# Optimization experiments

Hardware: AMD Instinct MI355X
Metric: run time of the kernel (lower is better)

Reference implementation:

```python
import jax, jax.numpy as jnp
import numpy as np

RCR, RCA = 5.1, 3.5
ETA_R, ZETA, ETA_A = 19.7, 14.1, 12.5
SHF_R = jnp.asarray((0.8 + 0.26875 * np.arange(16)).astype(np.float32))   # 16 radial shifts
SHF_Z = jnp.asarray(((2 * np.arange(8) + 1) * np.pi / 8).astype(np.float32))  # 8 angle shifts
SHF_A = jnp.asarray((0.8 + 0.3375 * np.arange(8)).astype(np.float32))    # 8 angular-radial shifts
NUM_SPECIES = 7
NUM_PAIRS = NUM_SPECIES * (NUM_SPECIES + 1) // 2  # 28 unordered species pairs
N = 2000          # atoms
K = 24            # max neighbors considered for angular terms (Rca=3.5 -> ~18 at this density)
BOX = 27.1        # (N / 0.1 atoms/A^3)^(1/3)

def _triu_index(n):
    ret = np.zeros((n, n), dtype=np.int32)
    iu = np.triu_indices(n)
    ret[iu] = np.arange(iu[0].size)
    ret[iu[1], iu[0]] = ret[iu]
    return ret
TRIU = jnp.asarray(_triu_index(NUM_SPECIES))  # [7,7] -> pair index in 0..27

def _fc(d, rc):
    # cosine cutoff, zero beyond rc
    return jnp.where(d <= rc, 0.5 * jnp.cos(jnp.pi * d / rc) + 0.5, 0.0)

def setup_inputs():
    key = jax.random.key(0)
    k1, k2 = jax.random.split(key)
    species = jax.random.randint(k1, (N,), 0, NUM_SPECIES)
    positions = jax.random.uniform(k2, (N, 3), dtype=jnp.float32) * BOX
    return {"species": species, "positions": positions}

def _aev_mean(species, positions):
    n = positions.shape[0]
    eye = jnp.eye(n, dtype=bool)
    diff = positions[:, None, :] - positions[None, :, :]          # [n,n,3]
    d2 = jnp.sum(diff * diff, -1)
    dist = jnp.sqrt(jnp.where(eye, 1.0, d2))                      # safe sqrt on diagonal
    dist = jnp.where(eye, 2.0 * RCR, dist)                        # exclude self (fc -> 0)

    # ---- radial AEV: 0.25 * exp(-EtaR (d - ShfR)^2) * fc(d, Rcr), scattered by neighbor species
    fc_r = _fc(dist, RCR)
    rad = 0.25 * jnp.exp(-ETA_R * (dist[..., None] - SHF_R) ** 2) * fc_r[..., None]  # [n,n,16]
    oh = jax.nn.one_hot(species, NUM_SPECIES, dtype=positions.dtype)                  # [n,7]
    radial = jnp.einsum('ijr,js->isr', rad, oh)                   # [n,7,16]

    # ---- angular AEV over triplets (j, i, k) with j,k among K nearest neighbors of i
    neg, idx = jax.lax.top_k(-dist, K)                            # idx: [n,K]
    nd = -neg                                                     # neighbor distances [n,K]
    valid = nd <= RCA
    vec = positions[idx] - positions[:, None, :]                  # [n,K,3]
    rj = nd[:, :, None]
    rk = nd[:, None, :]
    cos_ang = 0.95 * jnp.einsum('nad,nbd->nab', vec, vec) / (rj * rk)  # torchani's 0.95 factor
    theta = jnp.arccos(cos_ang)                                   # [n,K,K]
    f1 = ((1.0 + jnp.cos(theta[..., None] - SHF_Z)) / 2.0) ** ZETA               # [n,K,K,8]
    f2 = jnp.exp(-ETA_A * (((rj + rk) / 2.0)[..., None] - SHF_A) ** 2)           # [n,K,K,8]
    fcj = _fc(nd, RCA)
    tri = jnp.triu(jnp.ones((K, K), dtype=bool), 1)               # unordered pairs j<k
    mask = valid[:, :, None] & valid[:, None, :] & tri
    pref = 2.0 * fcj[:, :, None] * fcj[:, None, :] * mask.astype(positions.dtype)
    g = (f1[..., :, None] * f2[..., None, :]).reshape(n, K, K, 64) * pref[..., None]  # [n,K,K,64]
    sp_nb = species[idx]                                          # [n,K]
    pair_idx = TRIU[sp_nb[:, :, None], sp_nb[:, None, :]]         # [n,K,K] in 0..27
    row = jnp.arange(n)[:, None, None]
    angular = jnp.zeros((n, NUM_PAIRS, 64), dtype=positions.dtype).at[row, pair_idx].add(g)

    aev = jnp.concatenate([radial.reshape(n, -1), angular.reshape(n, -1)], axis=-1)  # [n,1904]
    return jnp.mean(aev)

def reference(species, positions):
    return _aev_mean(species, positions)
```

## Files before the change

kernel.cpp:

```cpp
#include <hip/hip_runtime.h>
#include <math.h>

#define NATOMS   2000
#define KNBR     24
#define CAND_CAP 64
#define BLOCK    256
#define NFEAT    1904.0f

__device__ __forceinline__ float wave_reduce_add(float v) {
    #pragma unroll
    for (int off = 32; off > 0; off >>= 1) v += __shfl_down(v, off, 64);
    return v;
}

__global__ __launch_bounds__(BLOCK) void aev_sum_kernel(
        const float* __restrict__ pos, float* __restrict__ accum) {
    constexpr float RCR = 5.1f, RCA = 3.5f;
    constexpr float ETA_R = 19.7f, ZETA = 14.1f, ETA_A = 12.5f;
    constexpr float PI = 3.14159265358979323846f;

    __shared__ float sx[NATOMS], sy[NATOMS], sz[NATOMS];
    __shared__ float cand_d[CAND_CAP];
    __shared__ int   cand_j[CAND_CAP];
    __shared__ int   s_cnt;
    __shared__ float nbx[KNBR], nby[KNBR], nbz[KNBR], nbd[KNBR], nbfc[KNBR];
    __shared__ float red_r[BLOCK / 64], red_a[BLOCK / 64];

    const int tid = threadIdx.x;
    const int i   = blockIdx.x;

    for (int j = tid; j < NATOMS; j += BLOCK) {
        sx[j] = pos[3 * j + 0];
        sy[j] = pos[3 * j + 1];
        sz[j] = pos[3 * j + 2];
    }
    if (tid == 0) s_cnt = 0;
    __syncthreads();

    const float xi = sx[i], yi = sy[i], zi = sz[i];

    float rsum = 0.0f;
    for (int j = tid; j < NATOMS; j += BLOCK) {
        if (j == i) continue;
        float dx = sx[j] - xi, dy = sy[j] - yi, dz = sz[j] - zi;
        float d2 = dx * dx + dy * dy + dz * dz;
        if (d2 <= RCR * RCR) {
            float d  = sqrtf(d2);
            float fc = 0.5f * __cosf(d * (PI / RCR)) + 0.5f;
            float s  = 0.0f;
            #pragma unroll
            for (int r = 0; r < 16; r++) {
                float t = d - (0.8f + 0.26875f * (float)r);
                s += __expf(-ETA_R * t * t);
            }
            rsum += 0.25f * fc * s;
            if (d2 <= RCA * RCA) {
                int c = atomicAdd(&s_cnt, 1);
                if (c < CAND_CAP) { cand_d[c] = d; cand_j[c] = j; }
            }
        }
    }
    rsum = wave_reduce_add(rsum);
    if ((tid & 63) == 0) red_r[tid >> 6] = rsum;
    __syncthreads();

    int cnt = min(s_cnt, CAND_CAP);
    int M   = min(cnt, KNBR);
    if (tid < cnt) {
        float dt = cand_d[tid];
        int   jt = cand_j[tid];
        int rank = 0;
        for (int u = 0; u < cnt; u++) {
            float du = cand_d[u];
            if (du < dt || (du == dt && cand_j[u] < jt)) rank++;
        }
        if (rank < KNBR) {
            nbx[rank]  = sx[jt] - xi;
            nby[rank]  = sy[jt] - yi;
            nbz[rank]  = sz[jt] - zi;
            nbd[rank]  = dt;
            nbfc[rank] = 0.5f * __cosf(dt * (PI / RCA)) + 0.5f;
        }
    }
    __syncthreads();

    float asum = 0.0f;
    int npairs = M * (M - 1) / 2;
    for (int p = tid; p < npairs; p += BLOCK) {
        int a = 0, rem = p;
        while (rem >= M - 1 - a) { rem -= M - 1 - a; a++; }
        int b = a + 1 + rem;

        float dot = nbx[a] * nbx[b] + nby[a] * nby[b] + nbz[a] * nbz[b];
        float ra = nbd[a], rb = nbd[b];
        float cosang = 0.95f * dot / (ra * rb);
        float theta  = acosf(cosang);

        float f1 = 0.0f;
        #pragma unroll
        for (int z = 0; z < 8; z++) {
            float shz = (2.0f * (float)z + 1.0f) * (PI / 8.0f);
            float c   = 0.5f * (1.0f + __cosf(theta - shz));
            f1 += __powf(fmaxf(c, 1e-20f), ZETA);
        }
        float avg = 0.5f * (ra + rb);
        float f2  = 0.0f;
        #pragma unroll
        for (int s8 = 0; s8 < 8; s8++) {
            float t = avg - (0.8f + 0.3375f * (float)s8);
            f2 += __expf(-ETA_A * t * t);
        }
        asum += 2.0f * nbfc[a] * nbfc[b] * f1 * f2;
    }
    asum = wave_reduce_add(asum);
    if ((tid & 63) == 0) red_a[tid >> 6] = asum;
    __syncthreads();

    if (tid == 0) {
        float total = 0.0f;
        #pragma unroll
        for (int w = 0; w < BLOCK / 64; w++) total += red_r[w] + red_a[w];
        atomicAdd(accum, total);
    }
}

__global__ void finalize_kernel(const float* __restrict__ accum,
                                float* __restrict__ out) {
    out[0] = accum[0] / ((float)NATOMS * NFEAT);
}

extern "C" void kernel_launch(void* const* d_in, const int* in_sizes, int n_in,
                              void* d_out, int out_size, void* d_ws, size_t ws_size,
                              hipStream_t stream) {
    const float* pos = (const float*)d_in[1];
    float* accum = (float*)d_ws;

    hipMemsetAsync(d_ws, 0, sizeof(float), stream);
    aev_sum_kernel<<<NATOMS, BLOCK, 0, stream>>>(pos, accum);
    finalize_kernel<<<1, 1, 0, stream>>>(accum, (float*)d_out);
}
```

Measured before the change: 96.47 us.

## Compact radial hits with wave ballot, drop shared position copy, per-block partials

```diff
diff --git a/kernel.cpp b/kernel.cpp
--- a/kernel.cpp
+++ b/kernel.cpp
@@ -3,7 +3,8 @@
 
 #define NATOMS   2000
 #define KNBR     24
-#define CAND_CAP 64
+#define HCAP     192
+#define ACAP     64
 #define BLOCK    256
 #define NFEAT    1904.0f
 
@@ -13,78 +14,89 @@
     return v;
 }
 
-__global__ __launch_bounds__(BLOCK) void aev_sum_kernel(
-        const float* __restrict__ pos, float* __restrict__ accum) {
+__global__ __launch_bounds__(BLOCK) void aev_block_kernel(
+        const float* __restrict__ pos, float* __restrict__ partial) {
     constexpr float RCR = 5.1f, RCA = 3.5f;
     constexpr float ETA_R = 19.7f, ZETA = 14.1f, ETA_A = 12.5f;
     constexpr float PI = 3.14159265358979323846f;
 
-    __shared__ float sx[NATOMS], sy[NATOMS], sz[NATOMS];
-    __shared__ float cand_d[CAND_CAP];
-    __shared__ int   cand_j[CAND_CAP];
-    __shared__ int   s_cnt;
+    __shared__ float hd2[HCAP];
+    __shared__ int   hj[HCAP];
+    __shared__ float ad[ACAP];
+    __shared__ int   aj[ACAP];
+    __shared__ int   s_hcnt, s_acnt;
     __shared__ float nbx[KNBR], nby[KNBR], nbz[KNBR], nbd[KNBR], nbfc[KNBR];
-    __shared__ float red_r[BLOCK / 64], red_a[BLOCK / 64];
+    __shared__ float red[BLOCK / 64];
 
-    const int tid = threadIdx.x;
-    const int i   = blockIdx.x;
+    const int tid  = threadIdx.x;
+    const int i    = blockIdx.x;
+    const int lane = tid & 63;
 
-    for (int j = tid; j < NATOMS; j += BLOCK) {
-        sx[j] = pos[3 * j + 0];
-        sy[j] = pos[3 * j + 1];
-        sz[j] = pos[3 * j + 2];
-    }
-    if (tid == 0) s_cnt = 0;
+    if (tid == 0) { s_hcnt = 0; s_acnt = 0; }
     __syncthreads();
 
-    const float xi = sx[i], yi = sy[i], zi = sz[i];
+    const float xi = pos[3 * i + 0], yi = pos[3 * i + 1], zi = pos[3 * i + 2];
 
-    float rsum = 0.0f;
-    for (int j = tid; j < NATOMS; j += BLOCK) {
-        if (j == i) continue;
-        float dx = sx[j] - xi, dy = sy[j] - yi, dz = sz[j] - zi;
+    for (int jb = 0; jb < NATOMS; jb += BLOCK) {
+        int j  = jb + tid;
+        int jc = j < NATOMS ? j : NATOMS - 1;
+        float dx = pos[3 * jc + 0] - xi;
+        float dy = pos[3 * jc + 1] - yi;
+        float dz = pos[3 * jc + 2] - zi;
         float d2 = dx * dx + dy * dy + dz * dz;
-        if (d2 <= RCR * RCR) {
-            float d  = sqrtf(d2);
-            float fc = 0.5f * __cosf(d * (PI / RCR)) + 0.5f;
-            float s  = 0.0f;
-            #pragma unroll
-            for (int r = 0; r < 16; r++) {
-                float t = d - (0.8f + 0.26875f * (float)r);
-                s += __expf(-ETA_R * t * t);
-            }
-            rsum += 0.25f * fc * s;
-            if (d2 <= RCA * RCA) {
-                int c = atomicAdd(&s_cnt, 1);
-                if (c < CAND_CAP) { cand_d[c] = d; cand_j[c] = j; }
-            }
+        bool hit = (j < NATOMS) && (j != i) && (d2 <= RCR * RCR);
+        unsigned long long m = __ballot(hit);
+        int nw   = __popcll(m);
+        int base = 0;
+        if (lane == 0 && nw) base = atomicAdd(&s_hcnt, nw);
+        base = __shfl(base, 0, 64);
+        if (hit) {
+            int idx = base + __popcll(m & ((1ull << lane) - 1ull));
+            if (idx < HCAP) { hd2[idx] = d2; hj[idx] = j; }
         }
     }
-    rsum = wave_reduce_add(rsum);
-    if ((tid & 63) == 0) red_r[tid >> 6] = rsum;
     __syncthreads();
 
-    int cnt = min(s_cnt, CAND_CAP);
+    float psum = 0.0f;
+    int hcnt = min(s_hcnt, HCAP);
+    for (int c = tid; c < hcnt; c += BLOCK) {
+        float d2 = hd2[c];
+        float d  = sqrtf(d2);
+        float fc = 0.5f * __cosf(d * (PI / RCR)) + 0.5f;
+        float s  = 0.0f;
+        #pragma unroll
+        for (int r = 0; r < 16; r++) {
+            float t = d - (0.8f + 0.26875f * (float)r);
+            s += __expf(-ETA_R * t * t);
+        }
+        psum += 0.25f * fc * s;
+        if (d2 <= RCA * RCA) {
+            int a = atomicAdd(&s_acnt, 1);
+            if (a < ACAP) { ad[a] = d; aj[a] = hj[c]; }
+        }
+    }
+    __syncthreads();
+
+    int cnt = min(s_acnt, ACAP);
     int M   = min(cnt, KNBR);
     if (tid < cnt) {
-        float dt = cand_d[tid];
-        int   jt = cand_j[tid];
+        float dt = ad[tid];
+        int   jt = aj[tid];
         int rank = 0;
         for (int u = 0; u < cnt; u++) {
-            float du = cand_d[u];
-            if (du < dt || (du == dt && cand_j[u] < jt)) rank++;
+            float du = ad[u];
+            if (du < dt || (du == dt && aj[u] < jt)) rank++;
         }
         if (rank < KNBR) {
-            nbx[rank]  = sx[jt] - xi;
-            nby[rank]  = sy[jt] - yi;
-            nbz[rank]  = sz[jt] - zi;
+            nbx[rank]  = pos[3 * jt + 0] - xi;
+            nby[rank]  = pos[3 * jt + 1] - yi;
+            nbz[rank]  = pos[3 * jt + 2] - zi;
             nbd[rank]  = dt;
             nbfc[rank] = 0.5f * __cosf(dt * (PI / RCA)) + 0.5f;
         }
     }
     __syncthreads();
 
-    float asum = 0.0f;
     int npairs = M * (M - 1) / 2;
     for (int p = tid; p < npairs; p += BLOCK) {
         int a = 0, rem = p;
@@ -110,32 +122,43 @@
             float t = avg - (0.8f + 0.3375f * (float)s8);
             f2 += __expf(-ETA_A * t * t);
         }
-        asum += 2.0f * nbfc[a] * nbfc[b] * f1 * f2;
+        psum += 2.0f * nbfc[a] * nbfc[b] * f1 * f2;
     }
-    asum = wave_reduce_add(asum);
-    if ((tid & 63) == 0) red_a[tid >> 6] = asum;
+
+    psum = wave_reduce_add(psum);
+    if (lane == 0) red[tid >> 6] = psum;
     __syncthreads();
-
     if (tid == 0) {
         float total = 0.0f;
         #pragma unroll
-        for (int w = 0; w < BLOCK / 64; w++) total += red_r[w] + red_a[w];
-        atomicAdd(accum, total);
+        for (int w = 0; w < BLOCK / 64; w++) total += red[w];
+        partial[i] = total;
     }
 }
 
-__global__ void finalize_kernel(const float* __restrict__ accum,
-                                float* __restrict__ out) {
-    out[0] = accum[0] / ((float)NATOMS * NFEAT);
+__global__ __launch_bounds__(BLOCK) void finalize_kernel(
+        const float* __restrict__ partial, float* __restrict__ out) {
+    __shared__ float red[BLOCK / 64];
+    const int tid = threadIdx.x;
+    float v = 0.0f;
+    for (int c = tid; c < NATOMS; c += BLOCK) v += partial[c];
+    v = wave_reduce_add(v);
+    if ((tid & 63) == 0) red[tid >> 6] = v;
+    __syncthreads();
+    if (tid == 0) {
+        float total = 0.0f;
+        #pragma unroll
+        for (int w = 0; w < BLOCK / 64; w++) total += red[w];
+        out[0] = total / ((float)NATOMS * NFEAT);
+    }
 }
 
 extern "C" void kernel_launch(void* const* d_in, const int* in_sizes, int n_in,
                               void* d_out, int out_size, void* d_ws, size_t ws_size,
                               hipStream_t stream) {
     const float* pos = (const float*)d_in[1];
-    float* accum = (float*)d_ws;
+    float* partial = (float*)d_ws;
 
-    hipMemsetAsync(d_ws, 0, sizeof(float), stream);
-    aev_sum_kernel<<<NATOMS, BLOCK, 0, stream>>>(pos, accum);
-    finalize_kernel<<<1, 1, 0, stream>>>(accum, (float*)d_out);
+    aev_block_kernel<<<NATOMS, BLOCK, 0, stream>>>(pos, partial);
+    finalize_kernel<<<1, BLOCK, 0, stream>>>(partial, (float*)d_out);
 }
```

Measured after the change: 78.62 us. 1.23x faster.
